# Kernel tuning notes

Measured on AMD Instinct MI355X. Metric: run time of the kernel, lower is better.

## Reference

```python
import jax, jax.numpy as jnp
import numpy as np

B, T, D, H, K = 64, 2000, 512, 256, 5


def setup_inputs() -> dict:
    key = jax.random.key(0)
    ks = jax.random.split(key, 4)
    state = jax.random.normal(ks[0], (B, 1, D), dtype=jnp.float32)
    enc_z = jax.random.normal(ks[1], (B, T, D), dtype=jnp.float32)
    # small init scale keeps exp(param_net(state)) numerically tame
    W1 = jax.random.normal(ks[2], (D, H), dtype=jnp.float32) * 0.05
    b1 = jnp.zeros((H,), dtype=jnp.float32)
    W2 = jax.random.normal(ks[3], (H, 3 * K), dtype=jnp.float32) * 0.05
    b2 = jnp.zeros((3 * K,), dtype=jnp.float32)
    return {"state": state, "enc_z": enc_z, "W1": W1, "b1": b1, "W2": W2, "b2": b2}


def reference(state, enc_z, W1, b1, W2, b2):
    # param_net: Linear -> Tanh -> Linear, then exp (all params positive)
    h = jnp.tanh(state @ W1 + b1)                 # [B,1,H]
    params = jnp.exp(h @ W2 + b2)                 # [B,1,3K]
    means = params[..., 0::3]                     # [B,1,K]  (gather of indices 3i)
    scales = params[..., 1::3]                    # [B,1,K]  (indices 3i+1)
    w = params[..., 2::3]                         # [B,1,K]  (indices 3i+2)
    # NOTE: original applies softmax over dim=1 (the singleton dim) -> all ones.
    weights = jax.nn.softmax(w, axis=1)           # [B,1,K] == ones (faithful)
    t = enc_z.shape[1]
    j = jnp.arange(t, dtype=enc_z.dtype)[None, :, None]  # [1,T,1]
    cdf = lambda x: jax.nn.sigmoid((x - means) / scales)  # broadcasts -> [B,T,K]
    probs = weights * (cdf(j + 0.5) - cdf(j - 0.5))        # [B,T,K]
    align = jnp.sum(probs, axis=2)                          # [B,T]
    context = jnp.einsum('bt,btd->bd', align, enc_z)[:, None, :]  # [B,1,D]
    return context
```

## Files before the change

kernel.cpp:

```cpp
#include <hip/hip_runtime.h>
#include <math.h>

#define BB 64
#define TT 2000
#define DD 512
#define HH 256
#define KK 5
#define PP (3*KK)
#define D4 (DD/4)
#define NSL 4
#define NJ 4


__global__ __launch_bounds__(256) void h_partial_kernel(
    const float* __restrict__ state,
    const float* __restrict__ W1,
    float* __restrict__ hpart)
{
    const int blk = blockIdx.x;
    const int b   = blk >> 2;
    const int s   = blk & 3;
    const int tid = threadIdx.x;
    const int q   = tid & 63;
    const int r   = tid >> 6;

    __shared__ float sst[128];
    __shared__ float s_part[4][HH];

    if (tid < 128) sst[tid] = state[(size_t)b * DD + s * 128 + tid];
    __syncthreads();

    const float4* w1v = (const float4*)W1;
    float4 acc = make_float4(0.f, 0.f, 0.f, 0.f);
    #pragma unroll 8
    for (int it = 0; it < 32; ++it) {
        const int dl = it * 4 + r;
        const int d  = s * 128 + dl;
        const float sv  = sst[dl];
        const float4 w  = w1v[(size_t)d * 64 + q];
        acc.x += sv * w.x; acc.y += sv * w.y;
        acc.z += sv * w.z; acc.w += sv * w.w;
    }
    s_part[r][4*q+0] = acc.x;
    s_part[r][4*q+1] = acc.y;
    s_part[r][4*q+2] = acc.z;
    s_part[r][4*q+3] = acc.w;
    __syncthreads();

    if (tid < HH)
        hpart[((size_t)b * NSL + s) * HH + tid] =
            s_part[0][tid] + s_part[1][tid] + s_part[2][tid] + s_part[3][tid];
}

__global__ __launch_bounds__(256) void context_kernel(
    const float* __restrict__ enc_z,
    const float* __restrict__ hpart,
    const float* __restrict__ b1,
    const float* __restrict__ W2,
    const float* __restrict__ b2,
    float* __restrict__ out)
{
    const int b   = blockIdx.x;
    const int j   = blockIdx.y;
    const int tid = threadIdx.x;
    const int h   = tid >> 5;
    const int c   = tid & 31;

    __shared__ float hs[HH];
    __shared__ float s_red[16][17];
    __shared__ float pr[PP];
    __shared__ float prm[16];
    __shared__ float al[TT];
    __shared__ float s_acc[8][128];

    {
        const float* hp = hpart + (size_t)b * NSL * HH + tid;
        hs[tid] = tanhf(b1[tid] + hp[0] + hp[HH] + hp[2*HH] + hp[3*HH]);
    }
    __syncthreads();

    {
        const int p = tid >> 4;
        const int g = tid & 15;
        float a = 0.f;
        if (p < PP) {
            #pragma unroll
            for (int i = 0; i < 16; ++i)
                a += hs[g + 16*i] * W2[(size_t)(g + 16*i) * PP + p];
        }
        s_red[p][g] = a;
    }
    __syncthreads();
    if (tid < PP) {
        float a = b2[tid];
        #pragma unroll
        for (int g = 0; g < 16; ++g) a += s_red[tid][g];
        pr[tid] = expf(a);
    }
    __syncthreads();
    if (tid == 0) {
        float tc = 1.0f;
        #pragma unroll
        for (int k = 0; k < KK; ++k)
            tc = fmaxf(tc, pr[3*k] + 36.0f * pr[3*k+1] + 1.0f);
        prm[15] = tc;
    }
    if (tid < KK) {
        prm[tid]     = pr[3*tid];
        prm[8 + tid] = 1.0f / pr[3*tid + 1];
    }
    __syncthreads();

    const int Tact = min(TT, (int)ceilf(prm[15]));
    for (int t = tid; t < Tact; t += 256) {
        const float tf = (float)t;
        float a = 0.0f;
        #pragma unroll
        for (int k = 0; k < KK; ++k) {
            const float m  = prm[k];
            const float is = prm[8 + k];
            const float hi = (tf + 0.5f - m) * is;
            const float lo = (tf - 0.5f - m) * is;
            a += 1.0f / (1.0f + expf(-hi)) - 1.0f / (1.0f + expf(-lo));
        }
        al[t] = a;
    }
    __syncthreads();

    const float4* e4 = (const float4*)enc_z + (size_t)b * TT * D4 + j * 32 + c;
    float ax = 0.f, ay = 0.f, az = 0.f, aw = 0.f;
    #pragma unroll 4
    for (int t = h; t < Tact; t += 8) {
        const float a  = al[t];
        const float4 v = e4[(size_t)t * D4];
        ax += a * v.x; ay += a * v.y; az += a * v.z; aw += a * v.w;
    }
    s_acc[h][4*c+0] = ax;
    s_acc[h][4*c+1] = ay;
    s_acc[h][4*c+2] = az;
    s_acc[h][4*c+3] = aw;
    __syncthreads();

    if (tid < 32) {
        float4 r = make_float4(0.f, 0.f, 0.f, 0.f);
        #pragma unroll
        for (int ph = 0; ph < 8; ++ph) {
            r.x += s_acc[ph][4*tid+0];
            r.y += s_acc[ph][4*tid+1];
            r.z += s_acc[ph][4*tid+2];
            r.w += s_acc[ph][4*tid+3];
        }
        ((float4*)out)[(size_t)b * D4 + j * 32 + tid] = r;
    }
}

extern "C" void kernel_launch(void* const* d_in, const int* in_sizes, int n_in,
                              void* d_out, int out_size, void* d_ws, size_t ws_size,
                              hipStream_t stream) {
    const float* state = (const float*)d_in[0];
    const float* enc_z = (const float*)d_in[1];
    const float* W1    = (const float*)d_in[2];
    const float* b1    = (const float*)d_in[3];
    const float* W2    = (const float*)d_in[4];
    const float* b2    = (const float*)d_in[5];
    float* out = (float*)d_out;

    float* ws_hpart = (float*)d_ws;

    h_partial_kernel<<<BB * NSL, 256, 0, stream>>>(state, W1, ws_hpart);
    context_kernel<<<dim3(BB, NJ), 256, 0, stream>>>(enc_z, ws_hpart, b1, W2, b2, out);
}
```

Baseline: 14.76 us.

## Fuse hidden-layer matvec into context kernel and widen blocks to 512 threads

Removes the separate h_partial kernel and its workspace round-trip. Each block of the context kernel now computes the full state@W1 product itself, using 8 slices of 64 rows reduced in shared memory. The grid shrinks to 64x2 blocks of 512 threads so each block covers 256 output columns. This saves a launch and the inter-kernel dependency, but every block redundantly reads all of W1 (512 KB per block) and runs the matvec serially before streaming enc_z, and fewer blocks are in flight.

```diff
diff --git a/kernel.cpp b/kernel.cpp
--- a/kernel.cpp
+++ b/kernel.cpp
@@ -8,53 +8,13 @@
 #define KK 5
 #define PP (3*KK)
 #define D4 (DD/4)
-#define NSL 4
-#define NJ 4
+#define NJ 2
 
 
-__global__ __launch_bounds__(256) void h_partial_kernel(
+__global__ __launch_bounds__(512) void molattn_fused_kernel(
     const float* __restrict__ state,
+    const float* __restrict__ enc_z,
     const float* __restrict__ W1,
-    float* __restrict__ hpart)
-{
-    const int blk = blockIdx.x;
-    const int b   = blk >> 2;
-    const int s   = blk & 3;
-    const int tid = threadIdx.x;
-    const int q   = tid & 63;
-    const int r   = tid >> 6;
-
-    __shared__ float sst[128];
-    __shared__ float s_part[4][HH];
-
-    if (tid < 128) sst[tid] = state[(size_t)b * DD + s * 128 + tid];
-    __syncthreads();
-
-    const float4* w1v = (const float4*)W1;
-    float4 acc = make_float4(0.f, 0.f, 0.f, 0.f);
-    #pragma unroll 8
-    for (int it = 0; it < 32; ++it) {
-        const int dl = it * 4 + r;
-        const int d  = s * 128 + dl;
-        const float sv  = sst[dl];
-        const float4 w  = w1v[(size_t)d * 64 + q];
-        acc.x += sv * w.x; acc.y += sv * w.y;
-        acc.z += sv * w.z; acc.w += sv * w.w;
-    }
-    s_part[r][4*q+0] = acc.x;
-    s_part[r][4*q+1] = acc.y;
-    s_part[r][4*q+2] = acc.z;
-    s_part[r][4*q+3] = acc.w;
-    __syncthreads();
-
-    if (tid < HH)
-        hpart[((size_t)b * NSL + s) * HH + tid] =
-            s_part[0][tid] + s_part[1][tid] + s_part[2][tid] + s_part[3][tid];
-}
-
-__global__ __launch_bounds__(256) void context_kernel(
-    const float* __restrict__ enc_z,
-    const float* __restrict__ hpart,
     const float* __restrict__ b1,
     const float* __restrict__ W2,
     const float* __restrict__ b2,
@@ -63,23 +23,48 @@
     const int b   = blockIdx.x;
     const int j   = blockIdx.y;
     const int tid = threadIdx.x;
-    const int h   = tid >> 5;
-    const int c   = tid & 31;
 
+    __shared__ float s_state[DD];
+    __shared__ float s_part[8][HH];
     __shared__ float hs[HH];
     __shared__ float s_red[16][17];
     __shared__ float pr[PP];
     __shared__ float prm[16];
     __shared__ float al[TT];
-    __shared__ float s_acc[8][128];
+    __shared__ float s_acc[8][256];
 
+    if (tid < DD) s_state[tid] = state[(size_t)b * DD + tid];
+    __syncthreads();
     {
-        const float* hp = hpart + (size_t)b * NSL * HH + tid;
-        hs[tid] = tanhf(b1[tid] + hp[0] + hp[HH] + hp[2*HH] + hp[3*HH]);
+        const int q  = tid & 63;
+        const int sl = tid >> 6;
+        const float4* w1v = (const float4*)W1;
+        const int d0 = sl * 64;
+        float4 acc = make_float4(0.f, 0.f, 0.f, 0.f);
+        #pragma unroll 16
+        for (int dd = 0; dd < 64; ++dd) {
+            const int d    = d0 + dd;
+            const float s  = s_state[d];
+            const float4 w = w1v[(size_t)d * 64 + q];
+            acc.x += s * w.x; acc.y += s * w.y;
+            acc.z += s * w.z; acc.w += s * w.w;
+        }
+        s_part[sl][4*q+0] = acc.x;
+        s_part[sl][4*q+1] = acc.y;
+        s_part[sl][4*q+2] = acc.z;
+        s_part[sl][4*q+3] = acc.w;
     }
     __syncthreads();
 
-    {
+    if (tid < HH) {
+        float a = b1[tid];
+        #pragma unroll
+        for (int s = 0; s < 8; ++s) a += s_part[s][tid];
+        hs[tid] = tanhf(a);
+    }
+    __syncthreads();
+
+    if (tid < 256) {
         const int p = tid >> 4;
         const int g = tid & 15;
         float a = 0.f;
@@ -112,7 +97,7 @@
     __syncthreads();
 
     const int Tact = min(TT, (int)ceilf(prm[15]));
-    for (int t = tid; t < Tact; t += 256) {
+    for (int t = tid; t < Tact; t += 512) {
         const float tf = (float)t;
         float a = 0.0f;
         #pragma unroll
@@ -127,21 +112,26 @@
     }
     __syncthreads();
 
-    const float4* e4 = (const float4*)enc_z + (size_t)b * TT * D4 + j * 32 + c;
-    float ax = 0.f, ay = 0.f, az = 0.f, aw = 0.f;
-    #pragma unroll 4
-    for (int t = h; t < Tact; t += 8) {
-        const float a  = al[t];
-        const float4 v = e4[(size_t)t * D4];
-        ax += a * v.x; ay += a * v.y; az += a * v.z; aw += a * v.w;
+    {
+        const int c = tid & 63;
+        const int h = tid >> 6;
+        const float4* e4 = (const float4*)enc_z
+                         + (size_t)b * TT * D4 + j * 64 + c;
+        float ax = 0.f, ay = 0.f, az = 0.f, aw = 0.f;
+        #pragma unroll 4
+        for (int t = h; t < Tact; t += 8) {
+            const float a  = al[t];
+            const float4 v = e4[(size_t)t * D4];
+            ax += a * v.x; ay += a * v.y; az += a * v.z; aw += a * v.w;
+        }
+        s_acc[h][4*c+0] = ax;
+        s_acc[h][4*c+1] = ay;
+        s_acc[h][4*c+2] = az;
+        s_acc[h][4*c+3] = aw;
     }
-    s_acc[h][4*c+0] = ax;
-    s_acc[h][4*c+1] = ay;
-    s_acc[h][4*c+2] = az;
-    s_acc[h][4*c+3] = aw;
     __syncthreads();
 
-    if (tid < 32) {
+    if (tid < 64) {
         float4 r = make_float4(0.f, 0.f, 0.f, 0.f);
         #pragma unroll
         for (int ph = 0; ph < 8; ++ph) {
@@ -150,7 +140,7 @@
             r.z += s_acc[ph][4*tid+2];
             r.w += s_acc[ph][4*tid+3];
         }
-        ((float4*)out)[(size_t)b * D4 + j * 32 + tid] = r;
+        ((float4*)out)[(size_t)b * D4 + j * 64 + tid] = r;
     }
 }
 
@@ -165,8 +155,6 @@
     const float* b2    = (const float*)d_in[5];
     float* out = (float*)d_out;
 
-    float* ws_hpart = (float*)d_ws;
-
-    h_partial_kernel<<<BB * NSL, 256, 0, stream>>>(state, W1, ws_hpart);
-    context_kernel<<<dim3(BB, NJ), 256, 0, stream>>>(enc_z, ws_hpart, b1, W2, b2, out);
+    molattn_fused_kernel<<<dim3(BB, NJ), 512, 0, stream>>>(
+        state, enc_z, W1, b1, W2, b2, out);
 }
```

Result: faster. 13.65 us (-7.5%).
